# Kernel tuning notes

Measured on AMD Instinct MI355X. Metric: run time of the kernel, lower is better.

Reference implementation:

```python
import jax, jax.numpy as jnp
import numpy as np

N_CONS = 100000
N_VARS = 200000
N_EDGES = 2000000
EMB = 64


def _emb(x, w0, b0, w1, b1):
    # Linear -> ReLU -> Linear -> ReLU
    h = jnp.maximum(x @ w0 + b0, 0.0)
    return jnp.maximum(h @ w1 + b1, 0.0)


def _bgc(left, src, dst, ef, right, lw, lb, ew, rw, fw, fb, ow0, ob0, ow1, ob1):
    # message: final(ReLU)(left_lin(right[dst]) + edge_lin(ef) + right_lin(left[src]))
    pre = right[dst] @ lw + lb + ef @ ew + left[src] @ rw          # [E, EMB]
    msg = jnp.maximum(pre, 0.0) @ fw + fb                          # [E, EMB]
    agg = jax.ops.segment_sum(msg, dst, num_segments=right.shape[0])  # [n_right, EMB]
    h = jnp.concatenate([agg, right], axis=-1)                     # [n_right, 2*EMB]
    return jnp.maximum(h @ ow0 + ob0, 0.0) @ ow1 + ob1


def setup_inputs() -> dict:
    key = jax.random.key(0)
    kit = iter(jax.random.split(key, 64))
    f32 = jnp.float32
    def W(i, o):
        return (jax.random.normal(next(kit), (i, o), f32) / np.float32(np.sqrt(i))).astype(f32)
    def B(o):
        return jnp.zeros((o,), f32)

    d = {}
    d['constraint_features'] = jax.random.normal(next(kit), (N_CONS, 5), f32)
    ei_c = jax.random.randint(next(kit), (N_EDGES,), 0, N_CONS)
    ei_v = jax.random.randint(next(kit), (N_EDGES,), 0, N_VARS)
    d['edge_indices'] = jnp.stack([ei_c, ei_v]).astype(jnp.int32)  # [2, E]
    d['edge_features'] = jax.random.normal(next(kit), (N_EDGES, 1), f32)
    d['variable_features'] = jax.random.normal(next(kit), (N_VARS, 19), f32)

    # cons / var embeddings
    d['cw0'], d['cb0'], d['cw1'], d['cb1'] = W(5, EMB), B(EMB), W(EMB, EMB), B(EMB)
    d['vw0'], d['vb0'], d['vw1'], d['vb1'] = W(19, EMB), B(EMB), W(EMB, EMB), B(EMB)
    # two bipartite convs
    for p in ('vc', 'cv'):
        d[p + '_lw'], d[p + '_lb'] = W(EMB, EMB), B(EMB)
        d[p + '_ew'] = W(1, EMB)
        d[p + '_rw'] = W(EMB, EMB)
        d[p + '_fw'], d[p + '_fb'] = W(EMB, EMB), B(EMB)
        d[p + '_ow0'], d[p + '_ob0'] = W(2 * EMB, EMB), B(EMB)
        d[p + '_ow1'], d[p + '_ob1'] = W(EMB, EMB), B(EMB)
    # policy head (final Linear has no bias)
    d['pw0'], d['pb0'], d['pw1'] = W(EMB, EMB), B(EMB), W(EMB, 1)
    # value head
    d['vhw0'], d['vhb0'], d['vhw1'], d['vhb1'] = W(EMB, EMB), B(EMB), W(EMB, 1), B(1)
    return d


def reference(constraint_features, edge_indices, edge_features, variable_features,
              cw0, cb0, cw1, cb1, vw0, vb0, vw1, vb1,
              vc_lw, vc_lb, vc_ew, vc_rw, vc_fw, vc_fb, vc_ow0, vc_ob0, vc_ow1, vc_ob1,
              cv_lw, cv_lb, cv_ew, cv_rw, cv_fw, cv_fb, cv_ow0, cv_ob0, cv_ow1, cv_ob1,
              pw0, pb0, pw1, vhw0, vhb0, vhw1, vhb1):
    cons_idx = edge_indices[0]
    var_idx = edge_indices[1]
    c = _emb(constraint_features, cw0, cb0, cw1, cb1)  # [n_cons, EMB]
    v = _emb(variable_features, vw0, vb0, vw1, vb1)    # [n_vars, EMB]
    # v -> c (reversed edges: src=var, dst=cons)
    c = _bgc(v, var_idx, cons_idx, edge_features, c,
             vc_lw, vc_lb, vc_ew, vc_rw, vc_fw, vc_fb, vc_ow0, vc_ob0, vc_ow1, vc_ob1)
    # c -> v (src=cons, dst=var)
    v = _bgc(c, cons_idx, var_idx, edge_features, v,
             cv_lw, cv_lb, cv_ew, cv_rw, cv_fw, cv_fb, cv_ow0, cv_ob0, cv_ow1, cv_ob1)
    policy = (jnp.maximum(v @ pw0 + pb0, 0.0) @ pw1).squeeze(-1)   # [n_vars]
    value = (jnp.maximum(v @ vhw0 + vhb0, 0.0) @ vhw1 + vhb1).squeeze(-1)  # [n_vars]
    return (value, policy)
```

## Files before the change

### kernel.cpp

```cpp
#include <hip/hip_runtime.h>

typedef unsigned short u16;

__device__ __forceinline__ float bf2f(u16 u) {
    return __uint_as_float(((unsigned int)u) << 16);
}
__device__ __forceinline__ u16 f2bf(float f) {
    unsigned int x = __float_as_uint(f);
    return (u16)((x + 0x7fffu + ((x >> 16) & 1u)) >> 16);
}


__device__ __forceinline__ void mm64(const float* A, const float* B, float* C, int lane)
{
    float bcol[64];
#pragma unroll
    for (int m = 0; m < 64; ++m) bcol[m] = B[m*64 + lane];
    for (int k = 0; k < 64; ++k) {
        float acc = 0.f;
#pragma unroll
        for (int m = 0; m < 64; ++m) acc = fmaf(A[k*64 + m], bcol[m], acc);
        C[k*64 + lane] = acc;
    }
}

__device__ __forceinline__ void vm64(const float* a, const float* B, const float* add,
                                     float* c, int lane)
{
    float acc = (add != 0) ? add[lane] : 0.f;
#pragma unroll
    for (int m = 0; m < 64; ++m) acc = fmaf(a[m], B[m*64 + lane], acc);
    c[lane] = acc;
}

__global__ __launch_bounds__(256) void prep_kernel(
    const float* vc_fw, const float* vc_fb, const float* vc_ow0,
    const float* vc_ow1, const float* vc_ob1,
    const float* cv_rw, const float* cv_fw, const float* cv_fb,
    const float* cv_ow0, const float* cv_ow1, const float* cv_ob1,
    const float* pw0, const float* pb0, const float* vhw0, const float* vhb0,
    float* Fc, float* gc, float* Hc, float* hc, float* Fv, float* gv,
    float* Pw, float* pbp, float* Vw, float* vbp)
{
    const int wv = threadIdx.x >> 6;
    const int lane = threadIdx.x & 63;
    if (wv == 0) {
        mm64(vc_fw, vc_ow0, Fc, lane);
        vm64(vc_fb, vc_ow0, 0, gc, lane);
    } else if (wv == 1) {
        mm64(vc_ow1, cv_rw, Hc, lane);
        vm64(vc_ob1, cv_rw, 0, hc, lane);
    } else if (wv == 2) {
        mm64(cv_fw, cv_ow0, Fv, lane);
        vm64(cv_fb, cv_ow0, 0, gv, lane);
    } else {
        mm64(cv_ow1, pw0, Pw, lane);
        vm64(cv_ob1, pw0, pb0, pbp, lane);
        mm64(cv_ow1, vhw0, Vw, lane);
        vm64(cv_ob1, vhw0, vhb0, vbp, lane);
    }
}

__global__ __launch_bounds__(256) void embc_kernel(
    const float* __restrict__ X,
    const float* __restrict__ W0, const float* __restrict__ B0,
    const float* __restrict__ W1, const float* __restrict__ B1,
    const float* __restrict__ LW, const float* __restrict__ LB,
    u16* __restrict__ c0out, float* __restrict__ RlOut, int M)
{
    const int lane = threadIdx.x & 63;
    const int wv   = threadIdx.x >> 6;
    __shared__ __align__(16) float xs[4][8*5];
    __shared__ __align__(16) float hb[4][8][64];
    __shared__ __align__(16) float yb[4][8][64];
    const int rowTile = (blockIdx.x*4 + wv)*8;

    for (int idx = lane; idx < 8*5; idx += 64) {
        long gi = (long)rowTile*5 + idx;
        xs[wv][idx] = (gi < (long)M*5) ? X[gi] : 0.f;
    }
    {
        float w0[5];
#pragma unroll
        for (int k = 0; k < 5; ++k) w0[k] = W0[k*64 + lane];
        const float b0 = B0[lane];
#pragma unroll
        for (int r = 0; r < 8; ++r) {
            float acc = b0;
#pragma unroll
            for (int k = 0; k < 5; ++k) acc = fmaf(xs[wv][r*5 + k], w0[k], acc);
            hb[wv][r][lane] = fmaxf(acc, 0.f);
        }
    }
    {
        float w1[64];
#pragma unroll
        for (int k = 0; k < 64; ++k) w1[k] = W1[k*64 + lane];
        const float b1 = B1[lane];
#pragma unroll
        for (int r = 0; r < 8; ++r) {
            float acc = b1;
#pragma unroll
            for (int k4 = 0; k4 < 16; ++k4) {
                float4 h4 = *(const float4*)&hb[wv][r][k4*4];
                acc = fmaf(h4.x, w1[k4*4+0], acc);
                acc = fmaf(h4.y, w1[k4*4+1], acc);
                acc = fmaf(h4.z, w1[k4*4+2], acc);
                acc = fmaf(h4.w, w1[k4*4+3], acc);
            }
            float y = fmaxf(acc, 0.f);
            yb[wv][r][lane] = y;
            int row = rowTile + r;
            if (row < M) c0out[(size_t)row*64 + lane] = f2bf(y);
        }
    }
    {
        float w[64];
#pragma unroll
        for (int k = 0; k < 64; ++k) w[k] = LW[k*64 + lane];
        const float bb = LB[lane];
#pragma unroll
        for (int r = 0; r < 8; ++r) {
            float acc = bb;
#pragma unroll
            for (int k4 = 0; k4 < 16; ++k4) {
                float4 y4 = *(const float4*)&yb[wv][r][k4*4];
                acc = fmaf(y4.x, w[k4*4+0], acc);
                acc = fmaf(y4.y, w[k4*4+1], acc);
                acc = fmaf(y4.z, w[k4*4+2], acc);
                acc = fmaf(y4.w, w[k4*4+3], acc);
            }
            int row = rowTile + r;
            if (row < M) RlOut[(size_t)row*64 + lane] = acc;
        }
    }
}

__global__ __launch_bounds__(256) void embv_kernel(
    const float* __restrict__ X,
    const float* __restrict__ W0, const float* __restrict__ B0,
    const float* __restrict__ W1, const float* __restrict__ B1,
    const float* __restrict__ RW,
    const float* __restrict__ LW, const float* __restrict__ LB,
    u16* __restrict__ v0out, u16* __restrict__ LsOut,
    float* __restrict__ RlOut, int M)
{
    const int lane = threadIdx.x & 63;
    const int wv   = threadIdx.x >> 6;
    __shared__ __align__(16) float xs[4][8*19];
    __shared__ __align__(16) float hb[4][8][64];
    __shared__ __align__(16) float yb[4][8][64];
    const int rowTile = (blockIdx.x*4 + wv)*8;

    for (int idx = lane; idx < 8*19; idx += 64) {
        long gi = (long)rowTile*19 + idx;
        xs[wv][idx] = (gi < (long)M*19) ? X[gi] : 0.f;
    }
    {
        float w0[19];
#pragma unroll
        for (int k = 0; k < 19; ++k) w0[k] = W0[k*64 + lane];
        const float b0 = B0[lane];
#pragma unroll
        for (int r = 0; r < 8; ++r) {
            float acc = b0;
#pragma unroll
            for (int k = 0; k < 19; ++k) acc = fmaf(xs[wv][r*19 + k], w0[k], acc);
            hb[wv][r][lane] = fmaxf(acc, 0.f);
        }
    }
    {
        float w1[64];
#pragma unroll
        for (int k = 0; k < 64; ++k) w1[k] = W1[k*64 + lane];
        const float b1 = B1[lane];
#pragma unroll
        for (int r = 0; r < 8; ++r) {
            float acc = b1;
#pragma unroll
            for (int k4 = 0; k4 < 16; ++k4) {
                float4 h4 = *(const float4*)&hb[wv][r][k4*4];
                acc = fmaf(h4.x, w1[k4*4+0], acc);
                acc = fmaf(h4.y, w1[k4*4+1], acc);
                acc = fmaf(h4.z, w1[k4*4+2], acc);
                acc = fmaf(h4.w, w1[k4*4+3], acc);
            }
            float y = fmaxf(acc, 0.f);
            yb[wv][r][lane] = y;
            int row = rowTile + r;
            if (row < M) v0out[(size_t)row*64 + lane] = f2bf(y);
        }
    }
    {
        float w[64];
#pragma unroll
        for (int k = 0; k < 64; ++k) w[k] = RW[k*64 + lane];
#pragma unroll
        for (int r = 0; r < 8; ++r) {
            float acc = 0.f;
#pragma unroll
            for (int k4 = 0; k4 < 16; ++k4) {
                float4 y4 = *(const float4*)&yb[wv][r][k4*4];
                acc = fmaf(y4.x, w[k4*4+0], acc);
                acc = fmaf(y4.y, w[k4*4+1], acc);
                acc = fmaf(y4.z, w[k4*4+2], acc);
                acc = fmaf(y4.w, w[k4*4+3], acc);
            }
            int row = rowTile + r;
            if (row < M) LsOut[(size_t)row*64 + lane] = f2bf(acc);
        }
    }
    {
        float w[64];
#pragma unroll
        for (int k = 0; k < 64; ++k) w[k] = LW[k*64 + lane];
        const float bb = LB[lane];
#pragma unroll
        for (int r = 0; r < 8; ++r) {
            float acc = bb;
#pragma unroll
            for (int k4 = 0; k4 < 16; ++k4) {
                float4 y4 = *(const float4*)&yb[wv][r][k4*4];
                acc = fmaf(y4.x, w[k4*4+0], acc);
                acc = fmaf(y4.y, w[k4*4+1], acc);
                acc = fmaf(y4.z, w[k4*4+2], acc);
                acc = fmaf(y4.w, w[k4*4+3], acc);
            }
            int row = rowTile + r;
            if (row < M) RlOut[(size_t)row*64 + lane] = acc;
        }
    }
}

__global__ __launch_bounds__(256) void hist2_kernel(
    const int* __restrict__ eic, const int* __restrict__ eiv,
    int* cntC, int* cntV, int E)
{
    int e = blockIdx.x*256 + threadIdx.x;
    if (e >= E) return;
    atomicAdd(&cntC[eic[e]], 1);
    atomicAdd(&cntV[eiv[e]], 1);
}

__global__ __launch_bounds__(256) void scan1_kernel(const int* __restrict__ in, int* blks, int N)
{
    __shared__ int sm[256];
    const int t = threadIdx.x;
    const int base = blockIdx.x*1024 + t*4;
    int s = 0;
#pragma unroll
    for (int i = 0; i < 4; ++i) { int idx = base + i; if (idx < N) s += in[idx]; }
    sm[t] = s; __syncthreads();
    for (int d = 128; d > 0; d >>= 1) { if (t < d) sm[t] += sm[t + d]; __syncthreads(); }
    if (t == 0) blks[blockIdx.x] = sm[0];
}

__global__ __launch_bounds__(256) void scan2_kernel(const int* __restrict__ blks, int* blkex, int nb)
{
    __shared__ int sm[1024];
    for (int i = threadIdx.x; i < nb; i += 256) sm[i] = blks[i];
    __syncthreads();
    if (threadIdx.x == 0) { int a = 0; for (int i = 0; i < nb; ++i) { int v = sm[i]; sm[i] = a; a += v; } }
    __syncthreads();
    for (int i = threadIdx.x; i < nb; i += 256) blkex[i] = sm[i];
}

__global__ __launch_bounds__(256) void scan3_kernel(
    const int* __restrict__ in, const int* __restrict__ blkex, int* out, int N)
{
    __shared__ int sm[256];
    const int t = threadIdx.x;
    const int base = blockIdx.x*1024 + t*4;
    int v[4]; int s = 0;
#pragma unroll
    for (int i = 0; i < 4; ++i) { int idx = base + i; v[i] = (idx < N) ? in[idx] : 0; s += v[i]; }
    sm[t] = s; __syncthreads();
    int x = s;
    for (int d = 1; d < 256; d <<= 1) {
        int y = (t >= d) ? sm[t - d] : 0;
        __syncthreads();
        x += y; sm[t] = x;
        __syncthreads();
    }
    int off0 = blkex[blockIdx.x] + (x - s);
#pragma unroll
    for (int i = 0; i < 4; ++i) {
        int idx = base + i;
        if (idx < N) {
            out[idx] = off0;
            off0 += v[i];
            if (idx == N - 1) out[N] = off0;
        }
    }
}

__global__ __launch_bounds__(256) void scatter1_kernel(
    const int* __restrict__ dIdx, const int* __restrict__ sIdx,
    const float* __restrict__ ef, int* cur, float2* __restrict__ bucket, int E)
{
    int e = blockIdx.x*256 + threadIdx.x;
    if (e >= E) return;
    int d = dIdx[e];
    int pos = atomicAdd(&cur[d], 1);
    bucket[pos] = make_float2(__int_as_float(sIdx[e]), ef[e]);
}

__global__ __launch_bounds__(256) void agg_kernel(
    const int* __restrict__ off, const float2* __restrict__ bucket,
    float* RlA, const u16* __restrict__ Lsb,
    const float* __restrict__ ew, int N)
{
    const int node = blockIdx.x*4 + (threadIdx.x >> 6);
    if (node >= N) return;
    const int lane = threadIdx.x & 63;
    const int s0 = off[node];
    const int e1 = off[node + 1];
    const float rl = RlA[(size_t)node*64 + lane];
    const float w  = ew[lane];

    float acc = 0.f;
    int j = s0;
    for (; j + 8 <= e1; j += 8) {
        float2 q0 = bucket[j+0], q1 = bucket[j+1], q2 = bucket[j+2], q3 = bucket[j+3];
        float2 q4 = bucket[j+4], q5 = bucket[j+5], q6 = bucket[j+6], q7 = bucket[j+7];
        float l0 = bf2f(Lsb[(size_t)__float_as_int(q0.x)*64 + lane]);
        float l1 = bf2f(Lsb[(size_t)__float_as_int(q1.x)*64 + lane]);
        float l2 = bf2f(Lsb[(size_t)__float_as_int(q2.x)*64 + lane]);
        float l3 = bf2f(Lsb[(size_t)__float_as_int(q3.x)*64 + lane]);
        float l4 = bf2f(Lsb[(size_t)__float_as_int(q4.x)*64 + lane]);
        float l5 = bf2f(Lsb[(size_t)__float_as_int(q5.x)*64 + lane]);
        float l6 = bf2f(Lsb[(size_t)__float_as_int(q6.x)*64 + lane]);
        float l7 = bf2f(Lsb[(size_t)__float_as_int(q7.x)*64 + lane]);
        acc += fmaxf(fmaf(q0.y, w, rl + l0), 0.f);
        acc += fmaxf(fmaf(q1.y, w, rl + l1), 0.f);
        acc += fmaxf(fmaf(q2.y, w, rl + l2), 0.f);
        acc += fmaxf(fmaf(q3.y, w, rl + l3), 0.f);
        acc += fmaxf(fmaf(q4.y, w, rl + l4), 0.f);
        acc += fmaxf(fmaf(q5.y, w, rl + l5), 0.f);
        acc += fmaxf(fmaf(q6.y, w, rl + l6), 0.f);
        acc += fmaxf(fmaf(q7.y, w, rl + l7), 0.f);
    }
    for (; j < e1; ++j) {
        float2 q = bucket[j];
        float l = bf2f(Lsb[(size_t)__float_as_int(q.x)*64 + lane]);
        acc += fmaxf(fmaf(q.y, w, rl + l), 0.f);
    }
    RlA[(size_t)node*64 + lane] = acc;
}

__global__ __launch_bounds__(256) void consupd_kernel(
    const float* __restrict__ aggpre, const u16* __restrict__ c0,
    const int* __restrict__ off,
    const float* __restrict__ Fc, const float* __restrict__ OW0B,
    const float* __restrict__ gc, const float* __restrict__ ob0,
    const float* __restrict__ Hc, const float* __restrict__ hc,
    u16* __restrict__ LsOut, int M)
{
    const int lane = threadIdx.x & 63;
    const int wv   = threadIdx.x >> 6;
    __shared__ __align__(16) float xs[4][8][64];
    __shared__ __align__(16) float cs[4][8][64];
    const int rowTile = (blockIdx.x*4 + wv)*8;

    float degv[8];
#pragma unroll
    for (int r = 0; r < 8; ++r) {
        int row = rowTile + r;
        int grow = (row < M) ? row : (M - 1);
        xs[wv][r][lane] = aggpre[(size_t)grow*64 + lane];
        cs[wv][r][lane] = bf2f(c0[(size_t)grow*64 + lane]);
        degv[r] = (float)(off[grow + 1] - off[grow]);
    }
    {
        float wa[64], wb[64];
#pragma unroll
        for (int k = 0; k < 64; ++k) { wa[k] = Fc[k*64 + lane]; wb[k] = OW0B[k*64 + lane]; }
        const float g_l = gc[lane], b_l = ob0[lane];
#pragma unroll
        for (int r = 0; r < 8; ++r) {
            float acc = fmaf(degv[r], g_l, b_l);
#pragma unroll
            for (int k4 = 0; k4 < 16; ++k4) {
                float4 x4 = *(const float4*)&xs[wv][r][k4*4];
                float4 c4 = *(const float4*)&cs[wv][r][k4*4];
                acc = fmaf(x4.x, wa[k4*4+0], acc); acc = fmaf(c4.x, wb[k4*4+0], acc);
                acc = fmaf(x4.y, wa[k4*4+1], acc); acc = fmaf(c4.y, wb[k4*4+1], acc);
                acc = fmaf(x4.z, wa[k4*4+2], acc); acc = fmaf(c4.z, wb[k4*4+2], acc);
                acc = fmaf(x4.w, wa[k4*4+3], acc); acc = fmaf(c4.w, wb[k4*4+3], acc);
            }
            xs[wv][r][lane] = fmaxf(acc, 0.f);
        }
    }
    {
        float wh[64];
#pragma unroll
        for (int k = 0; k < 64; ++k) wh[k] = Hc[k*64 + lane];
        const float h_l = hc[lane];
#pragma unroll
        for (int r = 0; r < 8; ++r) {
            float acc = h_l;
#pragma unroll
            for (int k4 = 0; k4 < 16; ++k4) {
                float4 u4 = *(const float4*)&xs[wv][r][k4*4];
                acc = fmaf(u4.x, wh[k4*4+0], acc);
                acc = fmaf(u4.y, wh[k4*4+1], acc);
                acc = fmaf(u4.z, wh[k4*4+2], acc);
                acc = fmaf(u4.w, wh[k4*4+3], acc);
            }
            int row = rowTile + r;
            if (row < M) LsOut[(size_t)row*64 + lane] = f2bf(acc);
        }
    }
}

__global__ __launch_bounds__(256) void varupdhead_kernel(
    const float* __restrict__ aggpre, const u16* __restrict__ v0,
    const int* __restrict__ off,
    const float* __restrict__ Fv, const float* __restrict__ OW0B,
    const float* __restrict__ gv, const float* __restrict__ ob0,
    const float* __restrict__ Pw, const float* __restrict__ pbp, const float* __restrict__ pw1,
    const float* __restrict__ Vw, const float* __restrict__ vbp, const float* __restrict__ vw1,
    const float* __restrict__ vb1,
    float* __restrict__ out, int M)
{
    const int lane = threadIdx.x & 63;
    const int wv   = threadIdx.x >> 6;
    __shared__ __align__(16) float xs[4][8][64];
    __shared__ __align__(16) float cs[4][8][64];
    const int rowTile = (blockIdx.x*4 + wv)*8;

    float degv[8];
#pragma unroll
    for (int r = 0; r < 8; ++r) {
        int row = rowTile + r;
        int grow = (row < M) ? row : (M - 1);
        xs[wv][r][lane] = aggpre[(size_t)grow*64 + lane];
        cs[wv][r][lane] = bf2f(v0[(size_t)grow*64 + lane]);
        degv[r] = (float)(off[grow + 1] - off[grow]);
    }
    {
        float wa[64], wb[64];
#pragma unroll
        for (int k = 0; k < 64; ++k) { wa[k] = Fv[k*64 + lane]; wb[k] = OW0B[k*64 + lane]; }
        const float g_l = gv[lane], b_l = ob0[lane];
#pragma unroll
        for (int r = 0; r < 8; ++r) {
            float acc = fmaf(degv[r], g_l, b_l);
#pragma unroll
            for (int k4 = 0; k4 < 16; ++k4) {
                float4 x4 = *(const float4*)&xs[wv][r][k4*4];
                float4 c4 = *(const float4*)&cs[wv][r][k4*4];
                acc = fmaf(x4.x, wa[k4*4+0], acc); acc = fmaf(c4.x, wb[k4*4+0], acc);
                acc = fmaf(x4.y, wa[k4*4+1], acc); acc = fmaf(c4.y, wb[k4*4+1], acc);
                acc = fmaf(x4.z, wa[k4*4+2], acc); acc = fmaf(c4.z, wb[k4*4+2], acc);
                acc = fmaf(x4.w, wa[k4*4+3], acc); acc = fmaf(c4.w, wb[k4*4+3], acc);
            }
            xs[wv][r][lane] = fmaxf(acc, 0.f);
        }
    }
    {
        float wp[64], wq[64];
#pragma unroll
        for (int k = 0; k < 64; ++k) { wp[k] = Pw[k*64 + lane]; wq[k] = Vw[k*64 + lane]; }
        const float pb_l = pbp[lane], vb_l = vbp[lane];
        const float p1w = pw1[lane], v1w = vw1[lane];
        const float vbias = vb1[0];
#pragma unroll
        for (int r = 0; r < 8; ++r) {
            float tp = pb_l, tv = vb_l;
#pragma unroll
            for (int k4 = 0; k4 < 16; ++k4) {
                float4 u4 = *(const float4*)&xs[wv][r][k4*4];
                tp = fmaf(u4.x, wp[k4*4+0], tp); tv = fmaf(u4.x, wq[k4*4+0], tv);
                tp = fmaf(u4.y, wp[k4*4+1], tp); tv = fmaf(u4.y, wq[k4*4+1], tv);
                tp = fmaf(u4.z, wp[k4*4+2], tp); tv = fmaf(u4.z, wq[k4*4+2], tv);
                tp = fmaf(u4.w, wp[k4*4+3], tp); tv = fmaf(u4.w, wq[k4*4+3], tv);
            }
            tp = fmaxf(tp, 0.f) * p1w;
            tv = fmaxf(tv, 0.f) * v1w;
#pragma unroll
            for (int m = 32; m >= 1; m >>= 1) {
                tp += __shfl_xor(tp, m, 64);
                tv += __shfl_xor(tv, m, 64);
            }
            int row = rowTile + r;
            if (lane == 0 && row < M) {
                out[row]     = tv + vbias;
                out[M + row] = tp;
            }
        }
    }
}

#define AL256(x) (((x) + 255) & ~(size_t)255)

extern "C" void kernel_launch(void* const* d_in, const int* in_sizes, int n_in,
                              void* d_out, int out_size, void* d_ws, size_t ws_size,
                              hipStream_t stream)
{
    const float* cf  = (const float*)d_in[0];
    const int*   ei  = (const int*)  d_in[1];
    const float* ef  = (const float*)d_in[2];
    const float* vf  = (const float*)d_in[3];

    const float* cw0 = (const float*)d_in[4];
    const float* cb0 = (const float*)d_in[5];
    const float* cw1 = (const float*)d_in[6];
    const float* cb1 = (const float*)d_in[7];
    const float* vw0 = (const float*)d_in[8];
    const float* vb0 = (const float*)d_in[9];
    const float* vw1 = (const float*)d_in[10];
    const float* vb1 = (const float*)d_in[11];

    const float* vc_lw  = (const float*)d_in[12];
    const float* vc_lb  = (const float*)d_in[13];
    const float* vc_ew  = (const float*)d_in[14];
    const float* vc_rw  = (const float*)d_in[15];
    const float* vc_fw  = (const float*)d_in[16];
    const float* vc_fb  = (const float*)d_in[17];
    const float* vc_ow0 = (const float*)d_in[18];
    const float* vc_ob0 = (const float*)d_in[19];
    const float* vc_ow1 = (const float*)d_in[20];
    const float* vc_ob1 = (const float*)d_in[21];

    const float* cv_lw  = (const float*)d_in[22];
    const float* cv_lb  = (const float*)d_in[23];
    const float* cv_ew  = (const float*)d_in[24];
    const float* cv_rw  = (const float*)d_in[25];
    const float* cv_fw  = (const float*)d_in[26];
    const float* cv_fb  = (const float*)d_in[27];
    const float* cv_ow0 = (const float*)d_in[28];
    const float* cv_ob0 = (const float*)d_in[29];
    const float* cv_ow1 = (const float*)d_in[30];
    const float* cv_ob1 = (const float*)d_in[31];

    const float* pw0  = (const float*)d_in[32];
    const float* pb0  = (const float*)d_in[33];
    const float* pw1  = (const float*)d_in[34];
    const float* vhw0 = (const float*)d_in[35];
    const float* vhb0 = (const float*)d_in[36];
    const float* vhw1 = (const float*)d_in[37];
    const float* vhb1 = (const float*)d_in[38];

    const int NC = in_sizes[0] / 5;
    const int E  = in_sizes[1] / 2;
    const int NV = in_sizes[3] / 19;
    const int* eic = ei;
    const int* eiv = ei + E;

    char* base = (char*)d_ws;
    size_t o = 0;
    float*  RlC = (float*)(base + o);  o += AL256((size_t)NC*64*4);
    u16*    c0b = (u16*)  (base + o);  o += AL256((size_t)NC*64*2);
    u16*    LsC = (u16*)  (base + o);  o += AL256((size_t)NC*64*2);
    float*  RlV = (float*)(base + o);  o += AL256((size_t)NV*64*4);
    u16*    v0b = (u16*)  (base + o);  o += AL256((size_t)NV*64*2);
    u16*    LsV = (u16*)  (base + o);  o += AL256((size_t)NV*64*2);
    float2* bkt = (float2*)(base + o); o += AL256((size_t)E*8);
    int* cntC = (int*)(base + o);  o += AL256((size_t)NC*4);
    int* offC = (int*)(base + o);  o += AL256(((size_t)NC + 1)*4);
    int* cntV = (int*)(base + o);  o += AL256((size_t)NV*4);
    int* offV = (int*)(base + o);  o += AL256(((size_t)NV + 1)*4);
    int* blks = (int*)(base + o);  o += AL256((size_t)1024*4);
    int* blkex= (int*)(base + o);  o += AL256((size_t)1024*4);
    float* Fc  = (float*)(base + o); o += AL256((size_t)4096*4);
    float* Hc  = (float*)(base + o); o += AL256((size_t)4096*4);
    float* Fv  = (float*)(base + o); o += AL256((size_t)4096*4);
    float* Pw  = (float*)(base + o); o += AL256((size_t)4096*4);
    float* Vw  = (float*)(base + o); o += AL256((size_t)4096*4);
    float* gc  = (float*)(base + o); o += AL256((size_t)64*4);
    float* hc  = (float*)(base + o); o += AL256((size_t)64*4);
    float* gv  = (float*)(base + o); o += AL256((size_t)64*4);
    float* pbp = (float*)(base + o); o += AL256((size_t)64*4);
    float* vbp = (float*)(base + o); o += AL256((size_t)64*4);

    if (o > ws_size) return;

    dim3 blk(256);
    dim3 gRowsC((unsigned)((NC + 31) / 32));
    dim3 gRowsV((unsigned)((NV + 31) / 32));
    dim3 gNodeC((unsigned)((NC + 3) / 4));
    dim3 gNodeV((unsigned)((NV + 3) / 4));
    dim3 gE((unsigned)((E + 255) / 256));
    const int nbC = (NC + 1023) / 1024;
    const int nbV = (NV + 1023) / 1024;

    (void)hipMemsetAsync(cntC, 0, (size_t)NC*4, stream);
    (void)hipMemsetAsync(cntV, 0, (size_t)NV*4, stream);
    hist2_kernel<<<gE, blk, 0, stream>>>(eic, eiv, cntC, cntV, E);
    scan1_kernel<<<dim3(nbC), blk, 0, stream>>>(cntC, blks, NC);
    scan2_kernel<<<dim3(1),   blk, 0, stream>>>(blks, blkex, nbC);
    scan3_kernel<<<dim3(nbC), blk, 0, stream>>>(cntC, blkex, offC, NC);
    scan1_kernel<<<dim3(nbV), blk, 0, stream>>>(cntV, blks, NV);
    scan2_kernel<<<dim3(1),   blk, 0, stream>>>(blks, blkex, nbV);
    scan3_kernel<<<dim3(nbV), blk, 0, stream>>>(cntV, blkex, offV, NV);

    prep_kernel<<<dim3(1), blk, 0, stream>>>(
        vc_fw, vc_fb, vc_ow0, vc_ow1, vc_ob1,
        cv_rw, cv_fw, cv_fb, cv_ow0, cv_ow1, cv_ob1,
        pw0, pb0, vhw0, vhb0,
        Fc, gc, Hc, hc, Fv, gv, Pw, pbp, Vw, vbp);

    embc_kernel<<<gRowsC, blk, 0, stream>>>(cf, cw0, cb0, cw1, cb1,
                                            vc_lw, vc_lb, c0b, RlC, NC);
    embv_kernel<<<gRowsV, blk, 0, stream>>>(vf, vw0, vb0, vw1, vb1,
                                            vc_rw, cv_lw, cv_lb, v0b, LsV, RlV, NV);

    (void)hipMemcpyAsync(cntC, offC, (size_t)NC*4, hipMemcpyDeviceToDevice, stream);
    scatter1_kernel<<<gE, blk, 0, stream>>>(eic, eiv, ef, cntC, bkt, E);
    agg_kernel<<<gNodeC, blk, 0, stream>>>(offC, bkt, RlC, LsV, vc_ew, NC);
    consupd_kernel<<<gRowsC, blk, 0, stream>>>(RlC, c0b, offC,
                                               Fc, vc_ow0 + 64*64, gc, vc_ob0,
                                               Hc, hc, LsC, NC);

    (void)hipMemcpyAsync(cntV, offV, (size_t)NV*4, hipMemcpyDeviceToDevice, stream);
    scatter1_kernel<<<gE, blk, 0, stream>>>(eiv, eic, ef, cntV, bkt, E);
    agg_kernel<<<gNodeV, blk, 0, stream>>>(offV, bkt, RlV, LsC, cv_ew, NV);
    varupdhead_kernel<<<gRowsV, blk, 0, stream>>>(RlV, v0b, offV,
                                                  Fv, cv_ow0 + 64*64, gv, cv_ob0,
                                                  Pw, pbp, pw1, Vw, vbp, vhw1, vhb1,
                                                  (float*)d_out, NV);
}
```

Baseline: 1.149 ms.

## Merge both edge scatters into one pass and retile node-update GEMMs

The two per-direction scatter kernels become a single scatter2 kernel. It reads edge indices and features once and fills separate constraint- and variable-side buckets, which costs an extra E*8-byte bucket buffer. The update and head kernels now process 16 rows per wave instead of 8. They hold one 64-entry weight column at a time with 16 accumulators, so each weight column is reused across more rows with fewer live weight registers. Launch bounds request 2 blocks per CU, and the larger shared-memory tiles may limit occupancy.

Result: slower. 3.396 ms (+195.6%).

```diff
diff --git a/kernel.cpp b/kernel.cpp
--- a/kernel.cpp
+++ b/kernel.cpp
@@ -294,15 +294,19 @@
     }
 }
 
-__global__ __launch_bounds__(256) void scatter1_kernel(
-    const int* __restrict__ dIdx, const int* __restrict__ sIdx,
-    const float* __restrict__ ef, int* cur, float2* __restrict__ bucket, int E)
+__global__ __launch_bounds__(256) void scatter2_kernel(
+    const int* __restrict__ eic, const int* __restrict__ eiv,
+    const float* __restrict__ ef,
+    int* curC, int* curV, float2* __restrict__ bC, float2* __restrict__ bV, int E)
 {
     int e = blockIdx.x*256 + threadIdx.x;
     if (e >= E) return;
-    int d = dIdx[e];
-    int pos = atomicAdd(&cur[d], 1);
-    bucket[pos] = make_float2(__int_as_float(sIdx[e]), ef[e]);
+    const int c = eic[e], v = eiv[e];
+    const float f = ef[e];
+    int pc = atomicAdd(&curC[c], 1);
+    bC[pc] = make_float2(__int_as_float(v), f);
+    int pv = atomicAdd(&curV[v], 1);
+    bV[pv] = make_float2(__int_as_float(c), f);
 }
 
 __global__ __launch_bounds__(256) void agg_kernel(
@@ -348,7 +352,7 @@
     RlA[(size_t)node*64 + lane] = acc;
 }
 
-__global__ __launch_bounds__(256) void consupd_kernel(
+__global__ __launch_bounds__(256, 2) void consupd_kernel(
     const float* __restrict__ aggpre, const u16* __restrict__ c0,
     const int* __restrict__ off,
     const float* __restrict__ Fc, const float* __restrict__ OW0B,
@@ -358,62 +362,81 @@
 {
     const int lane = threadIdx.x & 63;
     const int wv   = threadIdx.x >> 6;
-    __shared__ __align__(16) float xs[4][8][64];
-    __shared__ __align__(16) float cs[4][8][64];
-    const int rowTile = (blockIdx.x*4 + wv)*8;
-
-    float degv[8];
-#pragma unroll
-    for (int r = 0; r < 8; ++r) {
+    __shared__ __align__(16) float xs[4][16][64];
+    __shared__ __align__(16) float cs[4][16][64];
+    const int rowTile = (blockIdx.x*4 + wv)*16;
+
+    const float g_l = gc[lane], b_l = ob0[lane];
+    float acc[16];
+#pragma unroll
+    for (int r = 0; r < 16; ++r) {
         int row = rowTile + r;
         int grow = (row < M) ? row : (M - 1);
         xs[wv][r][lane] = aggpre[(size_t)grow*64 + lane];
         cs[wv][r][lane] = bf2f(c0[(size_t)grow*64 + lane]);
-        degv[r] = (float)(off[grow + 1] - off[grow]);
-    }
-    {
-        float wa[64], wb[64];
-#pragma unroll
-        for (int k = 0; k < 64; ++k) { wa[k] = Fc[k*64 + lane]; wb[k] = OW0B[k*64 + lane]; }
-        const float g_l = gc[lane], b_l = ob0[lane];
-#pragma unroll
-        for (int r = 0; r < 8; ++r) {
-            float acc = fmaf(degv[r], g_l, b_l);
-#pragma unroll
-            for (int k4 = 0; k4 < 16; ++k4) {
+        acc[r] = fmaf((float)(off[grow + 1] - off[grow]), g_l, b_l);
+    }
+    {
+        float w[64];
+#pragma unroll
+        for (int k = 0; k < 64; ++k) w[k] = Fc[k*64 + lane];
+#pragma unroll
+        for (int k4 = 0; k4 < 16; ++k4) {
+#pragma unroll
+            for (int r = 0; r < 16; ++r) {
                 float4 x4 = *(const float4*)&xs[wv][r][k4*4];
+                acc[r] = fmaf(x4.x, w[k4*4+0], acc[r]);
+                acc[r] = fmaf(x4.y, w[k4*4+1], acc[r]);
+                acc[r] = fmaf(x4.z, w[k4*4+2], acc[r]);
+                acc[r] = fmaf(x4.w, w[k4*4+3], acc[r]);
+            }
+        }
+    }
+    {
+        float w[64];
+#pragma unroll
+        for (int k = 0; k < 64; ++k) w[k] = OW0B[k*64 + lane];
+#pragma unroll
+        for (int k4 = 0; k4 < 16; ++k4) {
+#pragma unroll
+            for (int r = 0; r < 16; ++r) {
                 float4 c4 = *(const float4*)&cs[wv][r][k4*4];
-                acc = fmaf(x4.x, wa[k4*4+0], acc); acc = fmaf(c4.x, wb[k4*4+0], acc);
-                acc = fmaf(x4.y, wa[k4*4+1], acc); acc = fmaf(c4.y, wb[k4*4+1], acc);
-                acc = fmaf(x4.z, wa[k4*4+2], acc); acc = fmaf(c4.z, wb[k4*4+2], acc);
-                acc = fmaf(x4.w, wa[k4*4+3], acc); acc = fmaf(c4.w, wb[k4*4+3], acc);
-            }
-            xs[wv][r][lane] = fmaxf(acc, 0.f);
-        }
-    }
-    {
-        float wh[64];
-#pragma unroll
-        for (int k = 0; k < 64; ++k) wh[k] = Hc[k*64 + lane];
+                acc[r] = fmaf(c4.x, w[k4*4+0], acc[r]);
+                acc[r] = fmaf(c4.y, w[k4*4+1], acc[r]);
+                acc[r] = fmaf(c4.z, w[k4*4+2], acc[r]);
+                acc[r] = fmaf(c4.w, w[k4*4+3], acc[r]);
+            }
+        }
+    }
+#pragma unroll
+    for (int r = 0; r < 16; ++r) xs[wv][r][lane] = fmaxf(acc[r], 0.f);
+    {
+        float w[64];
+#pragma unroll
+        for (int k = 0; k < 64; ++k) w[k] = Hc[k*64 + lane];
         const float h_l = hc[lane];
 #pragma unroll
-        for (int r = 0; r < 8; ++r) {
-            float acc = h_l;
-#pragma unroll
-            for (int k4 = 0; k4 < 16; ++k4) {
+        for (int r = 0; r < 16; ++r) acc[r] = h_l;
+#pragma unroll
+        for (int k4 = 0; k4 < 16; ++k4) {
+#pragma unroll
+            for (int r = 0; r < 16; ++r) {
                 float4 u4 = *(const float4*)&xs[wv][r][k4*4];
-                acc = fmaf(u4.x, wh[k4*4+0], acc);
-                acc = fmaf(u4.y, wh[k4*4+1], acc);
-                acc = fmaf(u4.z, wh[k4*4+2], acc);
-                acc = fmaf(u4.w, wh[k4*4+3], acc);
-            }
+                acc[r] = fmaf(u4.x, w[k4*4+0], acc[r]);
+                acc[r] = fmaf(u4.y, w[k4*4+1], acc[r]);
+                acc[r] = fmaf(u4.z, w[k4*4+2], acc[r]);
+                acc[r] = fmaf(u4.w, w[k4*4+3], acc[r]);
+            }
+        }
+#pragma unroll
+        for (int r = 0; r < 16; ++r) {
             int row = rowTile + r;
-            if (row < M) LsOut[(size_t)row*64 + lane] = f2bf(acc);
-        }
-    }
-}
-
-__global__ __launch_bounds__(256) void varupdhead_kernel(
+            if (row < M) LsOut[(size_t)row*64 + lane] = f2bf(acc[r]);
+        }
+    }
+}
+
+__global__ __launch_bounds__(256, 2) void varupdhead_kernel(
     const float* __restrict__ aggpre, const u16* __restrict__ v0,
     const int* __restrict__ off,
     const float* __restrict__ Fv, const float* __restrict__ OW0B,
@@ -425,69 +448,109 @@
 {
     const int lane = threadIdx.x & 63;
     const int wv   = threadIdx.x >> 6;
-    __shared__ __align__(16) float xs[4][8][64];
-    __shared__ __align__(16) float cs[4][8][64];
-    const int rowTile = (blockIdx.x*4 + wv)*8;
-
-    float degv[8];
-#pragma unroll
-    for (int r = 0; r < 8; ++r) {
+    __shared__ __align__(16) float xs[4][16][64];
+    __shared__ __align__(16) float cs[4][16][64];
+    const int rowTile = (blockIdx.x*4 + wv)*16;
+
+    const float g_l = gv[lane], b_l = ob0[lane];
+    float acc[16];
+#pragma unroll
+    for (int r = 0; r < 16; ++r) {
         int row = rowTile + r;
         int grow = (row < M) ? row : (M - 1);
         xs[wv][r][lane] = aggpre[(size_t)grow*64 + lane];
         cs[wv][r][lane] = bf2f(v0[(size_t)grow*64 + lane]);
-        degv[r] = (float)(off[grow + 1] - off[grow]);
-    }
-    {
-        float wa[64], wb[64];
-#pragma unroll
-        for (int k = 0; k < 64; ++k) { wa[k] = Fv[k*64 + lane]; wb[k] = OW0B[k*64 + lane]; }
-        const float g_l = gv[lane], b_l = ob0[lane];
-#pragma unroll
-        for (int r = 0; r < 8; ++r) {
-            float acc = fmaf(degv[r], g_l, b_l);
-#pragma unroll
-            for (int k4 = 0; k4 < 16; ++k4) {
+        acc[r] = fmaf((float)(off[grow + 1] - off[grow]), g_l, b_l);
+    }
+    {
+        float w[64];
+#pragma unroll
+        for (int k = 0; k < 64; ++k) w[k] = Fv[k*64 + lane];
+#pragma unroll
+        for (int k4 = 0; k4 < 16; ++k4) {
+#pragma unroll
+            for (int r = 0; r < 16; ++r) {
                 float4 x4 = *(const float4*)&xs[wv][r][k4*4];
+                acc[r] = fmaf(x4.x, w[k4*4+0], acc[r]);
+                acc[r] = fmaf(x4.y, w[k4*4+1], acc[r]);
+                acc[r] = fmaf(x4.z, w[k4*4+2], acc[r]);
+                acc[r] = fmaf(x4.w, w[k4*4+3], acc[r]);
+            }
+        }
+    }
+    {
+        float w[64];
+#pragma unroll
+        for (int k = 0; k < 64; ++k) w[k] = OW0B[k*64 + lane];
+#pragma unroll
+        for (int k4 = 0; k4 < 16; ++k4) {
+#pragma unroll
+            for (int r = 0; r < 16; ++r) {
                 float4 c4 = *(const float4*)&cs[wv][r][k4*4];
-                acc = fmaf(x4.x, wa[k4*4+0], acc); acc = fmaf(c4.x, wb[k4*4+0], acc);
-                acc = fmaf(x4.y, wa[k4*4+1], acc); acc = fmaf(c4.y, wb[k4*4+1], acc);
-                acc = fmaf(x4.z, wa[k4*4+2], acc); acc = fmaf(c4.z, wb[k4*4+2], acc);
-                acc = fmaf(x4.w, wa[k4*4+3], acc); acc = fmaf(c4.w, wb[k4*4+3], acc);
-            }
-            xs[wv][r][lane] = fmaxf(acc, 0.f);
-        }
-    }
-    {
-        float wp[64], wq[64];
-#pragma unroll
-        for (int k = 0; k < 64; ++k) { wp[k] = Pw[k*64 + lane]; wq[k] = Vw[k*64 + lane]; }
-        const float pb_l = pbp[lane], vb_l = vbp[lane];
-        const float p1w = pw1[lane], v1w = vw1[lane];
-        const float vbias = vb1[0];
-#pragma unroll
-        for (int r = 0; r < 8; ++r) {
-            float tp = pb_l, tv = vb_l;
-#pragma unroll
-            for (int k4 = 0; k4 < 16; ++k4) {
+                acc[r] = fmaf(c4.x, w[k4*4+0], acc[r]);
+                acc[r] = fmaf(c4.y, w[k4*4+1], acc[r]);
+                acc[r] = fmaf(c4.z, w[k4*4+2], acc[r]);
+                acc[r] = fmaf(c4.w, w[k4*4+3], acc[r]);
+            }
+        }
+    }
+#pragma unroll
+    for (int r = 0; r < 16; ++r) xs[wv][r][lane] = fmaxf(acc[r], 0.f);
+
+    float tp[16];
+    {
+        float w[64];
+#pragma unroll
+        for (int k = 0; k < 64; ++k) w[k] = Pw[k*64 + lane];
+        const float pb_l = pbp[lane];
+#pragma unroll
+        for (int r = 0; r < 16; ++r) tp[r] = pb_l;
+#pragma unroll
+        for (int k4 = 0; k4 < 16; ++k4) {
+#pragma unroll
+            for (int r = 0; r < 16; ++r) {
                 float4 u4 = *(const float4*)&xs[wv][r][k4*4];
-                tp = fmaf(u4.x, wp[k4*4+0], tp); tv = fmaf(u4.x, wq[k4*4+0], tv);
-                tp = fmaf(u4.y, wp[k4*4+1], tp); tv = fmaf(u4.y, wq[k4*4+1], tv);
-                tp = fmaf(u4.z, wp[k4*4+2], tp); tv = fmaf(u4.z, wq[k4*4+2], tv);
-                tp = fmaf(u4.w, wp[k4*4+3], tp); tv = fmaf(u4.w, wq[k4*4+3], tv);
-            }
-            tp = fmaxf(tp, 0.f) * p1w;
-            tv = fmaxf(tv, 0.f) * v1w;
-#pragma unroll
-            for (int m = 32; m >= 1; m >>= 1) {
-                tp += __shfl_xor(tp, m, 64);
-                tv += __shfl_xor(tv, m, 64);
-            }
-            int row = rowTile + r;
-            if (lane == 0 && row < M) {
-                out[row]     = tv + vbias;
-                out[M + row] = tp;
-            }
+                tp[r] = fmaf(u4.x, w[k4*4+0], tp[r]);
+                tp[r] = fmaf(u4.y, w[k4*4+1], tp[r]);
+                tp[r] = fmaf(u4.z, w[k4*4+2], tp[r]);
+                tp[r] = fmaf(u4.w, w[k4*4+3], tp[r]);
+            }
+        }
+    }
+    {
+        float w[64];
+#pragma unroll
+        for (int k = 0; k < 64; ++k) w[k] = Vw[k*64 + lane];
+        const float vb_l = vbp[lane];
+#pragma unroll
+        for (int r = 0; r < 16; ++r) acc[r] = vb_l;
+#pragma unroll
+        for (int k4 = 0; k4 < 16; ++k4) {
+#pragma unroll
+            for (int r = 0; r < 16; ++r) {
+                float4 u4 = *(const float4*)&xs[wv][r][k4*4];
+                acc[r] = fmaf(u4.x, w[k4*4+0], acc[r]);
+                acc[r] = fmaf(u4.y, w[k4*4+1], acc[r]);
+                acc[r] = fmaf(u4.z, w[k4*4+2], acc[r]);
+                acc[r] = fmaf(u4.w, w[k4*4+3], acc[r]);
+            }
+        }
+    }
+    const float p1w = pw1[lane], v1w = vw1[lane];
+    const float vbias = vb1[0];
+#pragma unroll
+    for (int r = 0; r < 16; ++r) {
+        float a = fmaxf(tp[r],  0.f) * p1w;
+        float b = fmaxf(acc[r], 0.f) * v1w;
+#pragma unroll
+        for (int m = 32; m >= 1; m >>= 1) {
+            a += __shfl_xor(a, m, 64);
+            b += __shfl_xor(b, m, 64);
+        }
+        int row = rowTile + r;
+        if (lane == 0 && row < M) {
+            out[row]     = b + vbias;
+            out[M + row] = a;
         }
     }
 }
@@ -556,7 +619,8 @@
     float*  RlV = (float*)(base + o);  o += AL256((size_t)NV*64*4);
     u16*    v0b = (u16*)  (base + o);  o += AL256((size_t)NV*64*2);
     u16*    LsV = (u16*)  (base + o);  o += AL256((size_t)NV*64*2);
-    float2* bkt = (float2*)(base + o); o += AL256((size_t)E*8);
+    float2* bktC = (float2*)(base + o); o += AL256((size_t)E*8);
+    float2* bktV = (float2*)(base + o); o += AL256((size_t)E*8);
     int* cntC = (int*)(base + o);  o += AL256((size_t)NC*4);
     int* offC = (int*)(base + o);  o += AL256(((size_t)NC + 1)*4);
     int* cntV = (int*)(base + o);  o += AL256((size_t)NV*4);
@@ -579,6 +643,8 @@
     dim3 blk(256);
     dim3 gRowsC((unsigned)((NC + 31) / 32));
     dim3 gRowsV((unsigned)((NV + 31) / 32));
+    dim3 gUpdC((unsigned)((NC + 63) / 64));
+    dim3 gUpdV((unsigned)((NV + 63) / 64));
     dim3 gNodeC((unsigned)((NC + 3) / 4));
     dim3 gNodeV((unsigned)((NV + 3) / 4));
     dim3 gE((unsigned)((E + 255) / 256));
@@ -607,17 +673,17 @@
                                             vc_rw, cv_lw, cv_lb, v0b, LsV, RlV, NV);
 
     (void)hipMemcpyAsync(cntC, offC, (size_t)NC*4, hipMemcpyDeviceToDevice, stream);
-    scatter1_kernel<<<gE, blk, 0, stream>>>(eic, eiv, ef, cntC, bkt, E);
-    agg_kernel<<<gNodeC, blk, 0, stream>>>(offC, bkt, RlC, LsV, vc_ew, NC);
-    consupd_kernel<<<gRowsC, blk, 0, stream>>>(RlC, c0b, offC,
-                                               Fc, vc_ow0 + 64*64, gc, vc_ob0,
-                                               Hc, hc, LsC, NC);
-
     (void)hipMemcpyAsync(cntV, offV, (size_t)NV*4, hipMemcpyDeviceToDevice, stream);
-    scatter1_kernel<<<gE, blk, 0, stream>>>(eiv, eic, ef, cntV, bkt, E);
-    agg_kernel<<<gNodeV, blk, 0, stream>>>(offV, bkt, RlV, LsC, cv_ew, NV);
-    varupdhead_kernel<<<gRowsV, blk, 0, stream>>>(RlV, v0b, offV,
-                                                  Fv, cv_ow0 + 64*64, gv, cv_ob0,
-                                                  Pw, pbp, pw1, Vw, vbp, vhw1, vhb1,
-                                                  (float*)d_out, NV);
-}
+    scatter2_kernel<<<gE, blk, 0, stream>>>(eic, eiv, ef, cntC, cntV, bktC, bktV, E);
+
+    agg_kernel<<<gNodeC, blk, 0, stream>>>(offC, bktC, RlC, LsV, vc_ew, NC);
+    consupd_kernel<<<gUpdC, blk, 0, stream>>>(RlC, c0b, offC,
+                                              Fc, vc_ow0 + 64*64, gc, vc_ob0,
+                                              Hc, hc, LsC, NC);
+
+    agg_kernel<<<gNodeV, blk, 0, stream>>>(offV, bktV, RlV, LsC, cv_ew, NV);
+    varupdhead_kernel<<<gUpdV, blk, 0, stream>>>(RlV, v0b, offV,
+                                                 Fv, cv_ow0 + 64*64, gv, cv_ob0,
+                                                 Pw, pbp, pw1, Vw, vbp, vhw1, vhb1,
+                                                 (float*)d_out, NV);
+}
```
